# Performance work log

Measured on AMD Instinct MI355X. Metric: run time of the kernel, lower is better.

The kernel has to match this reference:

```python
import jax, jax.numpy as jnp
import numpy as np

B, N, DIN, DE, NH, DK = 4, 256, 128, 64, 8, 16


def setup_inputs() -> dict:
    key = jax.random.key(0)
    ks = jax.random.split(key, 8)
    s = 0.05
    return {
        "h": jax.random.normal(ks[0], (B, N, DIN), jnp.float32),
        "e": jax.random.normal(ks[1], (B, N, N, DE), jnp.float32),
        "mask": jnp.ones((B, N), jnp.float32),
        "WQ": jax.random.normal(ks[2], (DIN, NH * DK), jnp.float32) * s,
        "WK": jax.random.normal(ks[3], (DIN, NH * DK), jnp.float32) * s,
        "WV": jax.random.normal(ks[4], (DIN, NH * DK), jnp.float32) * s,
        "WE": jax.random.normal(ks[5], (DE, NH * DK), jnp.float32) * s,
        "WE2": jax.random.normal(ks[6], (DE, NH * DK), jnp.float32) * s,
    }


def reference(h, e, mask, WQ, WK, WV, WE, WE2):
    b, n, _ = h.shape
    Q = (h @ WQ).reshape(b, n, NH, DK)
    K = (h @ WK).reshape(b, n, NH, DK) * (float(DK) ** -0.5)
    V = (h @ WV).reshape(b, n, NH, DK)
    E = (e @ WE).reshape(b, n, n, NH, DK)
    E2 = (e @ WE2).reshape(b, n, n, NH, DK)
    # edge-augmented scores: (b, i, j, h, k)
    scores = jnp.einsum('bihk,bjhk->bijh', Q, K)[..., None] + E2
    scores = jnp.exp(jnp.clip(scores, -5.0, 5.0))
    attn_mask = mask[:, :, None, None, None] * mask[:, None, :, None, None]
    scores = scores * attn_mask
    softmax_denom = jnp.clip(scores.sum(axis=2), 1e-6, None)  # (b,i,h,k)
    scores = scores * attn_mask  # attn_dropout p=0.0 -> identity
    out = jnp.einsum('bijhk,bjhk->bihk', scores, V)
    out = out + (scores * E).sum(axis=2)
    out = out / softmax_denom
    return out.reshape(b, n, NH * DK)
```

## Files before the change

### kernel.cpp

```cpp
#include <hip/hip_runtime.h>

#define BB   4
#define NN   256
#define DIN  128
#define DE   64
#define NH   8
#define DK   16
#define CC   128

typedef __attribute__((ext_vector_type(8))) short short8;
typedef __attribute__((ext_vector_type(4))) float f32x4;

__device__ __forceinline__ unsigned short f2bfu(float f) {
    union { float f; unsigned int i; } v; v.f = f;
    unsigned int x = v.i;
    x += 0x7FFFu + ((x >> 16) & 1u);
    return (unsigned short)(x >> 16);
}

__global__ __launch_bounds__(256) void prep_kernel(
    const float* __restrict__ h, const float* __restrict__ WQ,
    const float* __restrict__ WK, const float* __restrict__ WV,
    const float* __restrict__ WE, const float* __restrict__ WE2,
    float* __restrict__ Qw, float* __restrict__ Kw, float* __restrict__ Vw,
    unsigned short* __restrict__ wfrag)
{
    __shared__ float hsh[4 * DIN];
    __shared__ float psum[4 * 1536];
    const int t = threadIdx.x;

    if (blockIdx.x >= 256) {
        const int tid  = (blockIdx.x - 256) * 256 + t;
        const int m    = tid >> 10;
        const int g    = (tid >> 7) & 7;
        const int ks   = (tid >> 6) & 1;
        const int lane = tid & 63;
        const int q4 = lane >> 4, l15 = lane & 15;
        const float* W = m ? WE2 : WE;
        union { uint4 u; unsigned short s[8]; } pk;
        #pragma unroll
        for (int ii = 0; ii < 8; ++ii) {
            const int d = ks * 32 + q4 * 8 + ii;
            pk.s[ii] = f2bfu(W[d * CC + g * 16 + l15]);
        }
        ((uint4*)wfrag)[tid] = pk.u;
        return;
    }

    const int r0 = blockIdx.x * 4;
    hsh[t]       = h[(size_t)r0 * DIN + t];
    hsh[256 + t] = h[(size_t)r0 * DIN + 256 + t];
    __syncthreads();

    const int cp  = t & 63;
    const int qtr = t >> 6;
    float aq[4][2], ak[4][2], av[4][2];
    #pragma unroll
    for (int r = 0; r < 4; ++r) {
        aq[r][0]=aq[r][1]=ak[r][0]=ak[r][1]=av[r][0]=av[r][1]=0.f;
    }
    #pragma unroll 4
    for (int dd = 0; dd < 32; ++dd) {
        const int d = qtr * 32 + dd;
        const float2 fq = ((const float2*)WQ)[d * 64 + cp];
        const float2 fk = ((const float2*)WK)[d * 64 + cp];
        const float2 fv = ((const float2*)WV)[d * 64 + cp];
        #pragma unroll
        for (int r = 0; r < 4; ++r) {
            const float hd = hsh[r * DIN + d];
            aq[r][0] = fmaf(hd, fq.x, aq[r][0]); aq[r][1] = fmaf(hd, fq.y, aq[r][1]);
            ak[r][0] = fmaf(hd, fk.x, ak[r][0]); ak[r][1] = fmaf(hd, fk.y, ak[r][1]);
            av[r][0] = fmaf(hd, fv.x, av[r][0]); av[r][1] = fmaf(hd, fv.y, av[r][1]);
        }
    }
    float* pq = psum + qtr * 1536;
    #pragma unroll
    for (int r = 0; r < 4; ++r) {
        pq[r*384       + 2*cp] = aq[r][0]; pq[r*384       + 2*cp+1] = aq[r][1];
        pq[r*384 + 128 + 2*cp] = ak[r][0]; pq[r*384 + 128 + 2*cp+1] = ak[r][1];
        pq[r*384 + 256 + 2*cp] = av[r][0]; pq[r*384 + 256 + 2*cp+1] = av[r][1];
    }
    __syncthreads();
    #pragma unroll
    for (int k = 0; k < 6; ++k) {
        const int o = k * 256 + t;
        float v = psum[o] + psum[1536 + o] + psum[3072 + o] + psum[4608 + o];
        const int r   = o / 384;
        const int mc  = o - r * 384;
        const int mat = mc >> 7;
        const int c   = mc & 127;
        const size_t idx = (size_t)(r0 + r) * CC + c;
        if      (mat == 0) Qw[idx] = v;
        else if (mat == 1) Kw[idx] = v * 0.25f;
        else               Vw[idx] = v;
    }
}

__global__ __launch_bounds__(512, 6) void attn_kernel(
    const float* __restrict__ e, const float* __restrict__ maskp,
    const unsigned short* __restrict__ wfrag,
    const float* __restrict__ Qw, const float* __restrict__ Kw,
    const float* __restrict__ Vw, float* __restrict__ out)
{
    __shared__ __align__(16) unsigned short esh[NN * DE];
    __shared__ float qk_sh[NN * 9];
    __shared__ float msk_sh[NN];
    __shared__ __align__(16) float qrow_sh[CC];

    const int row  = blockIdx.x;
    const int b    = row >> 8, i = row & 255;
    const int t    = threadIdx.x;
    const int wave = t >> 6, lane = t & 63;
    const int q4   = lane >> 4;
    const int l15  = lane & 15;

    {
        const f32x4* src = (const f32x4*)(e + (size_t)row * NN * DE);
        uint4* dst = (uint4*)esh;
        #pragma unroll
        for (int r = 0; r < 4; ++r) {
            const int cidx = r * 512 + t;
            const int j = cidx >> 3, ch = cidx & 7;
            const f32x4 f0 = __builtin_nontemporal_load(&src[2 * cidx]);
            const f32x4 f1 = __builtin_nontemporal_load(&src[2 * cidx + 1]);
            union { uint4 u; unsigned short s[8]; } pk;
            pk.s[0]=f2bfu(f0[0]); pk.s[1]=f2bfu(f0[1]); pk.s[2]=f2bfu(f0[2]); pk.s[3]=f2bfu(f0[3]);
            pk.s[4]=f2bfu(f1[0]); pk.s[5]=f2bfu(f1[1]); pk.s[6]=f2bfu(f1[2]); pk.s[7]=f2bfu(f1[3]);
            dst[j * 8 + (ch ^ (j & 7))] = pk.u;
        }
    }
    if (t < CC) qrow_sh[t] = Qw[(size_t)row * CC + t];
    if (t < NN) msk_sh[t] = maskp[b * NN + t];

    short8 bfragE[2], bfragS[2];
    {
        const uint4* wf = (const uint4*)wfrag;
        #pragma unroll
        for (int ks = 0; ks < 2; ++ks) {
            union { uint4 u; short8 s8; } cv;
            cv.u = wf[((0 * 8 + wave) * 2 + ks) * 64 + lane];
            bfragE[ks] = cv.s8;
            cv.u = wf[((1 * 8 + wave) * 2 + ks) * 64 + lane];
            bfragS[ks] = cv.s8;
        }
    }
    __syncthreads();

    {
        const int q = t & 31;
        const int hq = q >> 2;
        const float4 qv = ((const float4*)qrow_sh)[q];
        const float4* kb = (const float4*)(Kw + (size_t)b * NN * CC);
        #pragma unroll 4
        for (int it = 0; it < 16; ++it) {
            const int c = it * 512 + t;
            const int j = c >> 5;
            const float4 kv = kb[c];
            float p = kv.x * qv.x + kv.y * qv.y + kv.z * qv.z + kv.w * qv.w;
            p += __shfl_xor(p, 1);
            p += __shfl_xor(p, 2);
            if ((t & 3) == 0) qk_sh[j * 9 + hq] = p;
        }
    }
    __syncthreads();

    const float mi = msk_sh[i];
    float acc = 0.f, dnm = 0.f;
    const short8* ep = (const short8*)esh;
    const int g = wave;
    const float* vbase = Vw + (size_t)(b * NN + q4 * 4) * CC + g * 16 + l15;

    float va[4], vb2[4];
    #pragma unroll
    for (int r = 0; r < 4; ++r) va[r]  = vbase[(0 * 16 + r) * CC];
    #pragma unroll
    for (int r = 0; r < 4; ++r) vb2[r] = vbase[(1 * 16 + r) * CC];

    #pragma unroll
    for (int s = 0; s < 16; ++s) {
        float vc[4];
        if (s < 14) {
            #pragma unroll
            for (int r = 0; r < 4; ++r) vc[r] = vbase[((s + 2) * 16 + r) * CC];
        }

        const int ja = s * 16 + l15;
        const short8 a0 = ep[ja * 8 + ((q4    ) ^ (ja & 7))];
        const short8 a1 = ep[ja * 8 + ((q4 + 4) ^ (ja & 7))];

        float qk[4], mm[4], mm2[4];
        #pragma unroll
        for (int r = 0; r < 4; ++r) {
            const int jr = s * 16 + q4 * 4 + r;
            qk[r] = qk_sh[jr * 9 + g];
            const float m = mi * msk_sh[jr];
            mm[r] = m; mm2[r] = m * m;
        }

        f32x4 s2 = {0.f,0.f,0.f,0.f}, eE = {0.f,0.f,0.f,0.f};
        s2 = __builtin_amdgcn_mfma_f32_16x16x32_bf16(a0, bfragS[0], s2, 0,0,0);
        s2 = __builtin_amdgcn_mfma_f32_16x16x32_bf16(a1, bfragS[1], s2, 0,0,0);
        eE = __builtin_amdgcn_mfma_f32_16x16x32_bf16(a0, bfragE[0], eE, 0,0,0);
        eE = __builtin_amdgcn_mfma_f32_16x16x32_bf16(a1, bfragE[1], eE, 0,0,0);

        #pragma unroll
        for (int r = 0; r < 4; ++r) {
            float sc = qk[r] + s2[r];
            sc = fminf(5.f, fmaxf(-5.f, sc));
            const float p = __expf(sc);
            dnm += p * mm[r];
            acc = fmaf(p * mm2[r], va[r] + eE[r], acc);
        }

        #pragma unroll
        for (int r = 0; r < 4; ++r) {
            va[r] = vb2[r];
            if (s < 14) vb2[r] = vc[r];
        }
    }

    acc += __shfl_xor(acc, 16); acc += __shfl_xor(acc, 32);
    dnm += __shfl_xor(dnm, 16); dnm += __shfl_xor(dnm, 32);
    if (lane < 16) {
        out[(size_t)row * CC + g * 16 + lane] = acc / fmaxf(dnm, 1e-6f);
    }
}

extern "C" void kernel_launch(void* const* d_in, const int* in_sizes, int n_in,
                              void* d_out, int out_size, void* d_ws, size_t ws_size,
                              hipStream_t stream)
{
    const float* h    = (const float*)d_in[0];
    const float* e    = (const float*)d_in[1];
    const float* mask = (const float*)d_in[2];
    const float* WQ   = (const float*)d_in[3];
    const float* WK   = (const float*)d_in[4];
    const float* WV   = (const float*)d_in[5];
    const float* WE   = (const float*)d_in[6];
    const float* WE2  = (const float*)d_in[7];

    unsigned short* wfrag = (unsigned short*)d_ws;
    float* Qw = (float*)((char*)d_ws + 32768);
    float* Kw = Qw + BB * NN * CC;
    float* Vw = Kw + BB * NN * CC;

    prep_kernel<<<264, 256, 0, stream>>>(h, WQ, WK, WV, WE, WE2,
                                         Qw, Kw, Vw, wfrag);
    attn_kernel<<<BB*NN, 512, 0, stream>>>(e, mask, wfrag, Qw, Kw, Vw,
                                           (float*)d_out);
}
```

Baseline: 142.6 us.

## Preload all V values into registers and precompute mask products in shared memory

All 64 V values per thread are now loaded up front into registers behind a scheduling barrier, replacing the rolling two-step prefetch. The occupancy hint drops from 6 to 4 blocks per CU so the larger register footprint fits. Mask products mi*mj and their squares are precomputed into two shared arrays, which removes per-iteration multiplies, and the denominator update becomes an fma. The aim is to hide global load latency for V, at the cost of fewer resident waves and more register pressure.

```diff
diff --git a/kernel.cpp b/kernel.cpp
--- a/kernel.cpp
+++ b/kernel.cpp
@@ -96,7 +96,7 @@
     }
 }
 
-__global__ __launch_bounds__(512, 6) void attn_kernel(
+__global__ __launch_bounds__(512, 4) void attn_kernel(
     const float* __restrict__ e, const float* __restrict__ maskp,
     const unsigned short* __restrict__ wfrag,
     const float* __restrict__ Qw, const float* __restrict__ Kw,
@@ -104,7 +104,8 @@
 {
     __shared__ __align__(16) unsigned short esh[NN * DE];
     __shared__ float qk_sh[NN * 9];
-    __shared__ float msk_sh[NN];
+    __shared__ float msk1_sh[NN];
+    __shared__ float msk2_sh[NN];
     __shared__ __align__(16) float qrow_sh[CC];
 
     const int row  = blockIdx.x;
@@ -130,7 +131,14 @@
         }
     }
     if (t < CC) qrow_sh[t] = Qw[(size_t)row * CC + t];
-    if (t < NN) msk_sh[t] = maskp[b * NN + t];
+    {
+        const float mi = maskp[b * NN + i];
+        if (t < NN) {
+            const float m1 = mi * maskp[b * NN + t];
+            msk1_sh[t] = m1;
+            msk2_sh[t] = m1 * m1;
+        }
+    }
 
     short8 bfragE[2], bfragS[2];
     {
@@ -164,37 +172,35 @@
     }
     __syncthreads();
 
-    const float mi = msk_sh[i];
+    const int g = wave;
+
+    const float* vbase = Vw + (size_t)(b * NN + q4 * 4) * CC + g * 16 + l15;
+    float vr[16][4];
+    #pragma unroll
+    for (int s = 0; s < 16; ++s) {
+        #pragma unroll
+        for (int r = 0; r < 4; ++r) {
+            vr[s][r] = vbase[(s * 16 + r) * CC];
+        }
+    }
+    __builtin_amdgcn_sched_barrier(0);
+
     float acc = 0.f, dnm = 0.f;
     const short8* ep = (const short8*)esh;
-    const int g = wave;
-    const float* vbase = Vw + (size_t)(b * NN + q4 * 4) * CC + g * 16 + l15;
-
-    float va[4], vb2[4];
-    #pragma unroll
-    for (int r = 0; r < 4; ++r) va[r]  = vbase[(0 * 16 + r) * CC];
-    #pragma unroll
-    for (int r = 0; r < 4; ++r) vb2[r] = vbase[(1 * 16 + r) * CC];
 
     #pragma unroll
     for (int s = 0; s < 16; ++s) {
-        float vc[4];
-        if (s < 14) {
-            #pragma unroll
-            for (int r = 0; r < 4; ++r) vc[r] = vbase[((s + 2) * 16 + r) * CC];
-        }
-
         const int ja = s * 16 + l15;
         const short8 a0 = ep[ja * 8 + ((q4    ) ^ (ja & 7))];
         const short8 a1 = ep[ja * 8 + ((q4 + 4) ^ (ja & 7))];
 
-        float qk[4], mm[4], mm2[4];
+        float qk[4], m1[4], m2[4];
         #pragma unroll
         for (int r = 0; r < 4; ++r) {
             const int jr = s * 16 + q4 * 4 + r;
             qk[r] = qk_sh[jr * 9 + g];
-            const float m = mi * msk_sh[jr];
-            mm[r] = m; mm2[r] = m * m;
+            m1[r] = msk1_sh[jr];
+            m2[r] = msk2_sh[jr];
         }
 
         f32x4 s2 = {0.f,0.f,0.f,0.f}, eE = {0.f,0.f,0.f,0.f};
@@ -208,14 +214,8 @@
             float sc = qk[r] + s2[r];
             sc = fminf(5.f, fmaxf(-5.f, sc));
             const float p = __expf(sc);
-            dnm += p * mm[r];
-            acc = fmaf(p * mm2[r], va[r] + eE[r], acc);
-        }
-
-        #pragma unroll
-        for (int r = 0; r < 4; ++r) {
-            va[r] = vb2[r];
-            if (s < 14) vb2[r] = vc[r];
+            dnm = fmaf(p, m1[r], dnm);
+            acc = fmaf(p * m2[r], vr[s][r] + eE[r], acc);
         }
     }
 
```

New measurement: 144.2 us. No clear change (+1.1%).
